# Optimization experiments

Hardware: AMD Instinct MI355X
Metric: run time of the kernel (lower is better)

The kernel has to match this reference:

```python
import jax, jax.numpy as jnp
import numpy as np

EPS = 1e-8  # torch cosine_similarity norm clamp


def _l2_normalize(x):
    # normalize last dim with torch-style eps clamp on the norm
    n = jnp.linalg.norm(x, axis=-1, keepdims=True)
    return x / jnp.maximum(n, EPS)


def setup_inputs() -> dict:
    key = jax.random.key(0)
    ks = jax.random.split(key, 6)
    T, Nq, D = 4, 4096, 1024
    Ns, H, P, C = 2048, 3, 256, 100
    return {
        "query_tube_feats": jax.random.normal(ks[0], (T, Nq, D), jnp.float32),
        "support_feats": jax.random.normal(ks[1], (Ns, D), jnp.float32),
        "head_W": jax.random.normal(ks[2], (H, D, P), jnp.float32) * (1.0 / np.sqrt(D)),
        "head_b": jax.random.normal(ks[3], (H, P), jnp.float32) * 0.01,
        "cls_W": jax.random.normal(ks[4], (D, C), jnp.float32) * (1.0 / np.sqrt(D)),
        "cls_b": jax.random.normal(ks[5], (C,), jnp.float32) * 0.01,
    }


def reference(query_tube_feats, support_feats, head_W, head_b, cls_W, cls_b):
    # aggregate_features with 'mean' aggregation over the tube/frame axis
    agg_query = jnp.mean(query_tube_feats, axis=0)                 # [Nq, D]

    # all 3 relation heads at once: Linear projections
    q = jnp.einsum('nd,hdp->hnp', agg_query, head_W) + head_b[:, None, :]   # [H, Nq, P]
    s = jnp.einsum('md,hdp->hmp', support_feats, head_W) + head_b[:, None, :]  # [H, Ns, P]

    # cosine similarity as fused normalize + GEMM (same math as broadcast cosine)
    qn = _l2_normalize(q)
    sn = _l2_normalize(s)
    dists = jnp.einsum('hnp,hmp->hnm', qn, sn)                     # [H, Nq, Ns]

    match_scores = jnp.mean(dists, axis=0)                         # [Nq, Ns]
    support_preds = support_feats @ cls_W + cls_b                  # [Ns, C]
    return match_scores, support_preds
```

## Files before the change

### kernel.cpp

```cpp
#include <hip/hip_runtime.h>

#define NQ 4096
#define NS 2048
#define DD 1024
#define HH 3
#define PP 256
#define CC 100
#define NR (NQ + NS)
#define PN (HH * PP)

typedef __attribute__((ext_vector_type(8))) short bf16x8;
typedef __attribute__((ext_vector_type(4))) float f32x4;

#define AS1 __attribute__((address_space(1)))
#define AS3 __attribute__((address_space(3)))

__device__ __forceinline__ void gload16(const void* g, void* l) {
  __builtin_amdgcn_global_load_lds((const AS1 unsigned int*)g,
                                   (AS3 unsigned int*)l, 16, 0, 0);
}

__device__ __forceinline__ unsigned short f2bf(float f) {
  union { float f; unsigned u; } v; v.f = f;
  return (unsigned short)((v.u + 0x7FFFu + ((v.u >> 16) & 1u)) >> 16);
}

__device__ __forceinline__ float bf2f(unsigned short s) {
  union { unsigned u; float f; } v; v.u = ((unsigned)s) << 16;
  return v.f;
}

__global__ __launch_bounds__(256) void prep_kernel(
    const float* __restrict__ q,
    const float* __restrict__ sup,
    const float* __restrict__ hW,
    const float* __restrict__ cW,
    unsigned short* __restrict__ Xq,
    unsigned short* __restrict__ Xs,
    unsigned short* __restrict__ Wt,
    unsigned short* __restrict__ WcT)
{
  __shared__ unsigned short T[64][72];
  const int b = blockIdx.x, t = threadIdx.x;

  if (b < 1536) {
    if (b < 1024) {
      #pragma unroll
      for (int i = 0; i < 4; ++i) {
        int idx = (b * 1024 + i * 256 + t) * 4;
        const float4 a  = *(const float4*)&q[idx];
        const float4 c1 = *(const float4*)&q[NQ * DD + idx];
        const float4 c2 = *(const float4*)&q[2 * NQ * DD + idx];
        const float4 c3 = *(const float4*)&q[3 * NQ * DD + idx];
        ushort4 o;
        o.x = f2bf((a.x + c1.x + c2.x + c3.x) * 0.25f);
        o.y = f2bf((a.y + c1.y + c2.y + c3.y) * 0.25f);
        o.z = f2bf((a.z + c1.z + c2.z + c3.z) * 0.25f);
        o.w = f2bf((a.w + c1.w + c2.w + c3.w) * 0.25f);
        *(ushort4*)&Xq[idx] = o;
      }
    } else {
      #pragma unroll
      for (int i = 0; i < 4; ++i) {
        int idx = ((b - 1024) * 1024 + i * 256 + t) * 4;
        const float4 a = *(const float4*)&sup[idx];
        ushort4 o;
        o.x = f2bf(a.x); o.y = f2bf(a.y); o.z = f2bf(a.z); o.w = f2bf(a.w);
        *(ushort4*)&Xs[idx] = o;
      }
    }
    return;
  }

  const float* src; unsigned short* dst; int srcC, pvalid, k0, p0;
  if (b < 1728) {
    int r = b - 1536; int h = r / 64; int rr = r % 64;
    k0 = (rr >> 2) * 64; p0 = (rr & 3) * 64;
    src = hW + h * DD * PP; srcC = PP; pvalid = PP;
    dst = Wt + (h * PP + p0) * DD;
  } else {
    int r = b - 1728;
    k0 = (r >> 1) * 64; p0 = (r & 1) * 64;
    src = cW; srcC = CC; pvalid = CC;
    dst = WcT + p0 * DD;
  }
  {
    int kl = t >> 2, pb = (t & 3) * 4;
    #pragma unroll
    for (int j = 0; j < 4; ++j) {
      int pl = pb + j * 16;
      int p = p0 + pl;
      float4 v; v.x = v.y = v.z = v.w = 0.f;
      if (p + 3 < pvalid) {
        v = *(const float4*)&src[(k0 + kl) * srcC + p];
      } else {
        if (p + 0 < pvalid) v.x = src[(k0 + kl) * srcC + p + 0];
        if (p + 1 < pvalid) v.y = src[(k0 + kl) * srcC + p + 1];
        if (p + 2 < pvalid) v.z = src[(k0 + kl) * srcC + p + 2];
        if (p + 3 < pvalid) v.w = src[(k0 + kl) * srcC + p + 3];
      }
      T[kl][pl + 0] = f2bf(v.x); T[kl][pl + 1] = f2bf(v.y);
      T[kl][pl + 2] = f2bf(v.z); T[kl][pl + 3] = f2bf(v.w);
    }
    __syncthreads();
    int pr = t >> 2, kb = (t & 3) * 4;
    #pragma unroll
    for (int j = 0; j < 4; ++j) {
      int kk = kb + j * 16;
      ushort4 o;
      o.x = T[kk + 0][pr]; o.y = T[kk + 1][pr];
      o.z = T[kk + 2][pr]; o.w = T[kk + 3][pr];
      *(ushort4*)&dst[pr * DD + k0 + kk] = o;
    }
  }
}

__global__ __launch_bounds__(256) void pgemm_kernel(
    const unsigned short* __restrict__ X,
    const unsigned short* __restrict__ Wall,
    const float* __restrict__ ball,
    unsigned short* __restrict__ QS)
{
  __shared__ __align__(16) char smem[65536];
  unsigned short* As = (unsigned short*)smem;
  unsigned short* Bs = (unsigned short*)(smem + 32768);
  unsigned short* Ct = (unsigned short*)smem;

  const int bid = blockIdx.x;
  const int swz = (bid & 7) * 36 + (bid >> 3);
  const int bm = swz / 6, bn = swz % 6;
  const int tid = threadIdx.x;
  const int w = tid >> 6, l = tid & 63;
  const int wm = w >> 1, wn = w & 1;
  const int rA = l & 15, kg = l >> 4;

  const unsigned short* A = X + bm * 128 * DD;
  const unsigned short* B = Wall + bn * 128 * DD;

  auto STAGE = [&](int buf, int kt) {
    #pragma unroll
    for (int i = 0; i < 8; ++i) {
      int c = w + i * 4;
      if (c < 16)
        gload16(A + (c * 8 + (l >> 3)) * DD + kt * 64 + (l & 7) * 8,
                &As[buf * 8192 + c * 512]);
      else
        gload16(B + ((c - 16) * 8 + (l >> 3)) * DD + kt * 64 + (l & 7) * 8,
                &Bs[buf * 8192 + (c - 16) * 512]);
    }
  };

  f32x4 acc[4][4] = {};
  STAGE(0, 0);
  __syncthreads();
  int cur = 0;
  for (int kt = 0; kt < DD / 64; ++kt) {
    if (kt + 1 < DD / 64) STAGE(cur ^ 1, kt + 1);
    #pragma unroll
    for (int kk = 0; kk < 2; ++kk) {
      bf16x8 a[4], bfr[4];
      #pragma unroll
      for (int mi = 0; mi < 4; ++mi)
        a[mi] = *(const bf16x8*)&As[cur * 8192 + (wm * 64 + mi * 16 + rA) * 64 + kk * 32 + kg * 8];
      #pragma unroll
      for (int ni = 0; ni < 4; ++ni)
        bfr[ni] = *(const bf16x8*)&Bs[cur * 8192 + (wn * 64 + ni * 16 + rA) * 64 + kk * 32 + kg * 8];
      #pragma unroll
      for (int mi = 0; mi < 4; ++mi)
        #pragma unroll
        for (int ni = 0; ni < 4; ++ni)
          acc[mi][ni] =
              __builtin_amdgcn_mfma_f32_16x16x32_bf16(a[mi], bfr[ni], acc[mi][ni], 0, 0, 0);
    }
    __syncthreads();
    cur ^= 1;
  }

  float bias[4];
  #pragma unroll
  for (int ni = 0; ni < 4; ++ni)
    bias[ni] = ball[bn * 128 + wn * 64 + ni * 16 + rA];

  #pragma unroll
  for (int mi = 0; mi < 4; ++mi)
    #pragma unroll
    for (int i = 0; i < 4; ++i) {
      int row = wm * 64 + mi * 16 + kg * 4 + i;
      #pragma unroll
      for (int ni = 0; ni < 4; ++ni)
        Ct[row * 136 + wn * 64 + ni * 16 + rA] = f2bf(acc[mi][ni][i] + bias[ni]);
    }
  __syncthreads();
  #pragma unroll
  for (int pass = 0; pass < 16; ++pass) {
    int row = pass * 8 + (tid >> 5);
    int c = tid & 31;
    ushort4 v = *(const ushort4*)&Ct[row * 136 + c * 4];
    *(ushort4*)&QS[(bm * 128 + row) * PN + bn * 128 + c * 4] = v;
  }
}

__global__ __launch_bounds__(256) void norm_kernel(
    unsigned short* __restrict__ QS)
{
  const int wid = blockIdx.x * 4 + (threadIdx.x >> 6);
  const int l = threadIdx.x & 63;
  unsigned short* rowp = QS + wid * PN;
  const float scale = (wid < NQ) ? (1.f / 3.f) : 1.f;

  float v[3][4];
  float ss[3];
  #pragma unroll
  for (int h = 0; h < 3; ++h) {
    ushort4 u = *(const ushort4*)&rowp[h * PP + l * 4];
    v[h][0] = bf2f(u.x); v[h][1] = bf2f(u.y);
    v[h][2] = bf2f(u.z); v[h][3] = bf2f(u.w);
    ss[h] = v[h][0]*v[h][0] + v[h][1]*v[h][1] + v[h][2]*v[h][2] + v[h][3]*v[h][3];
  }
  #pragma unroll
  for (int s = 1; s < 64; s <<= 1) {
    ss[0] += __shfl_xor(ss[0], s);
    ss[1] += __shfl_xor(ss[1], s);
    ss[2] += __shfl_xor(ss[2], s);
  }
  #pragma unroll
  for (int h = 0; h < 3; ++h) {
    float inv = scale / fmaxf(sqrtf(ss[h]), 1e-8f);
    ushort4 o;
    o.x = f2bf(v[h][0] * inv); o.y = f2bf(v[h][1] * inv);
    o.z = f2bf(v[h][2] * inv); o.w = f2bf(v[h][3] * inv);
    *(ushort4*)&rowp[h * PP + l * 4] = o;
  }
}

__global__ __launch_bounds__(256) void mm_kernel(
    const unsigned short* __restrict__ Qn,
    const unsigned short* __restrict__ Sn,
    const unsigned short* __restrict__ Xs,
    const unsigned short* __restrict__ WcT,
    const float* __restrict__ cb,
    float* __restrict__ out)
{
  __shared__ __align__(16) char smem[128 * 132 * 4];
  unsigned short* As = (unsigned short*)smem;
  unsigned short* Bs = (unsigned short*)(smem + 32768);
  float* Ct = (float*)smem;

  const int bid = blockIdx.x;
  const int tid = threadIdx.x;
  const int w = tid >> 6, l = tid & 63;
  const int wm = w >> 1, wn = w & 1;
  const int rA = l & 15, kg = l >> 4;

  const unsigned short *A, *B;
  int ldk, nkt, bm, bn;
  const bool match = bid < 512;
  if (match) {
    int xcd = bid & 7, idx = bid >> 3;
    bm = xcd * 4 + (idx & 3);
    bn = idx >> 2;
    A = Qn + bm * 128 * PN;
    B = Sn + bn * 128 * PN;
    ldk = PN; nkt = PN / 64;
  } else {
    bm = bid - 512; bn = 0;
    A = Xs + bm * 128 * DD;
    B = WcT;
    ldk = DD; nkt = DD / 64;
  }

  auto STAGE = [&](int buf, int kt) {
    #pragma unroll
    for (int i = 0; i < 8; ++i) {
      int c = w + i * 4;
      if (c < 16)
        gload16(A + (c * 8 + (l >> 3)) * ldk + kt * 64 + (l & 7) * 8,
                &As[buf * 8192 + c * 512]);
      else
        gload16(B + ((c - 16) * 8 + (l >> 3)) * ldk + kt * 64 + (l & 7) * 8,
                &Bs[buf * 8192 + (c - 16) * 512]);
    }
  };

  f32x4 acc[4][4] = {};
  STAGE(0, 0);
  __syncthreads();
  int cur = 0;
  for (int kt = 0; kt < nkt; ++kt) {
    if (kt + 1 < nkt) STAGE(cur ^ 1, kt + 1);
    #pragma unroll
    for (int kk = 0; kk < 2; ++kk) {
      bf16x8 a[4], bfr[4];
      #pragma unroll
      for (int mi = 0; mi < 4; ++mi)
        a[mi] = *(const bf16x8*)&As[cur * 8192 + (wm * 64 + mi * 16 + rA) * 64 + kk * 32 + kg * 8];
      #pragma unroll
      for (int ni = 0; ni < 4; ++ni)
        bfr[ni] = *(const bf16x8*)&Bs[cur * 8192 + (wn * 64 + ni * 16 + rA) * 64 + kk * 32 + kg * 8];
      #pragma unroll
      for (int mi = 0; mi < 4; ++mi)
        #pragma unroll
        for (int ni = 0; ni < 4; ++ni)
          acc[mi][ni] =
              __builtin_amdgcn_mfma_f32_16x16x32_bf16(a[mi], bfr[ni], acc[mi][ni], 0, 0, 0);
    }
    __syncthreads();
    cur ^= 1;
  }

  if (match) {
    #pragma unroll
    for (int mi = 0; mi < 4; ++mi)
      #pragma unroll
      for (int i = 0; i < 4; ++i) {
        int row = wm * 64 + mi * 16 + kg * 4 + i;
        #pragma unroll
        for (int ni = 0; ni < 4; ++ni)
          Ct[row * 132 + wn * 64 + ni * 16 + rA] = acc[mi][ni][i];
      }
    __syncthreads();
    #pragma unroll
    for (int pass = 0; pass < 16; ++pass) {
      int row = pass * 8 + (tid >> 5);
      int c = tid & 31;
      f32x4 v = *(const f32x4*)&Ct[row * 132 + c * 4];
      *(f32x4*)&out[(long)(bm * 128 + row) * NS + bn * 128 + c * 4] = v;
    }
  } else {
    float* o2 = out + (long)NQ * NS;
    #pragma unroll
    for (int mi = 0; mi < 4; ++mi)
      #pragma unroll
      for (int i = 0; i < 4; ++i) {
        int row = bm * 128 + wm * 64 + mi * 16 + kg * 4 + i;
        #pragma unroll
        for (int ni = 0; ni < 4; ++ni) {
          int col = wn * 64 + ni * 16 + rA;
          if (col < CC) o2[row * CC + col] = acc[mi][ni][i] + cb[col];
        }
      }
  }
}

extern "C" void kernel_launch(void* const* d_in, const int* in_sizes, int n_in,
                              void* d_out, int out_size, void* d_ws, size_t ws_size,
                              hipStream_t stream) {
  const float* q   = (const float*)d_in[0];
  const float* sup = (const float*)d_in[1];
  const float* hW  = (const float*)d_in[2];
  const float* hb  = (const float*)d_in[3];
  const float* cW  = (const float*)d_in[4];
  const float* cb  = (const float*)d_in[5];
  float* out = (float*)d_out;

  char* ws = (char*)d_ws;
  unsigned short* Xq  = (unsigned short*)(ws + 0);
  unsigned short* Xs  = (unsigned short*)(ws + (8u  << 20));
  unsigned short* Wt  = (unsigned short*)(ws + (12u << 20));
  unsigned short* WcT = (unsigned short*)(ws + (12u << 20) + 1572864u);
  unsigned short* QS  = (unsigned short*)(ws + (14u << 20));
  unsigned short* Qn  = QS;
  unsigned short* Sn  = QS + (size_t)NQ * PN;

  prep_kernel<<<1760, 256, 0, stream>>>(q, sup, hW, cW, Xq, Xs, Wt, WcT);
  pgemm_kernel<<<288, 256, 0, stream>>>(Xq, Wt, hb, QS);
  norm_kernel<<<NR / 4, 256, 0, stream>>>(QS);
  mm_kernel<<<512 + 16, 256, 0, stream>>>(Qn, Sn, Xs, WcT, cb, out);
}
```

Before: 181.7 us.

## XOR-swizzle LDS tiles and use explicit vmcnt waits for async pipelining

Both GEMM kernels now load global tiles into LDS with the column position XOR-swizzled by row, and read fragments back with the matching XOR. This is meant to remove LDS bank conflicts on the fragment reads. The loop also replaces __syncthreads with explicit s_waitcnt vmcnt(8) plus raw s_barrier, so the prefetch of the next tile can stay in flight while the current tile is consumed. The hand-placed waitcnt values depend on exactly eight loads per stage; if the count is wrong the kernel may read incomplete data.

```diff
diff --git a/kernel.cpp b/kernel.cpp
--- a/kernel.cpp
+++ b/kernel.cpp
@@ -14,6 +14,9 @@
 
 #define AS1 __attribute__((address_space(1)))
 #define AS3 __attribute__((address_space(3)))
+
+#define S_WAIT_VM(n) asm volatile("s_waitcnt vmcnt(" #n ")" ::: "memory")
+#define S_WAIT_LGKM0() asm volatile("s_waitcnt lgkmcnt(0)" ::: "memory")
 
 __device__ __forceinline__ void gload16(const void* g, void* l) {
   __builtin_amdgcn_global_load_lds((const AS1 unsigned int*)g,
@@ -133,6 +136,8 @@
   const int w = tid >> 6, l = tid & 63;
   const int wm = w >> 1, wn = w & 1;
   const int rA = l & 15, kg = l >> 4;
+  const int xr = (rA & 7) << 3;
+  const int colsw = ((l & 7) * 8) ^ ((l >> 3) << 3);
 
   const unsigned short* A = X + bm * 128 * DD;
   const unsigned short* B = Wall + bn * 128 * DD;
@@ -142,29 +147,37 @@
     for (int i = 0; i < 8; ++i) {
       int c = w + i * 4;
       if (c < 16)
-        gload16(A + (c * 8 + (l >> 3)) * DD + kt * 64 + (l & 7) * 8,
+        gload16(A + (c * 8 + (l >> 3)) * DD + kt * 64 + colsw,
                 &As[buf * 8192 + c * 512]);
       else
-        gload16(B + ((c - 16) * 8 + (l >> 3)) * DD + kt * 64 + (l & 7) * 8,
+        gload16(B + ((c - 16) * 8 + (l >> 3)) * DD + kt * 64 + colsw,
                 &Bs[buf * 8192 + (c - 16) * 512]);
     }
   };
 
   f32x4 acc[4][4] = {};
   STAGE(0, 0);
-  __syncthreads();
   int cur = 0;
   for (int kt = 0; kt < DD / 64; ++kt) {
-    if (kt + 1 < DD / 64) STAGE(cur ^ 1, kt + 1);
+    if (kt + 1 < DD / 64) {
+      STAGE(cur ^ 1, kt + 1);
+      S_WAIT_VM(8);
+    } else {
+      S_WAIT_VM(0);
+    }
+    __builtin_amdgcn_sched_barrier(0);
+    __builtin_amdgcn_s_barrier();
     #pragma unroll
     for (int kk = 0; kk < 2; ++kk) {
       bf16x8 a[4], bfr[4];
       #pragma unroll
       for (int mi = 0; mi < 4; ++mi)
-        a[mi] = *(const bf16x8*)&As[cur * 8192 + (wm * 64 + mi * 16 + rA) * 64 + kk * 32 + kg * 8];
+        a[mi] = *(const bf16x8*)&As[cur * 8192 + (wm * 64 + mi * 16 + rA) * 64 +
+                                    ((kk * 32 + kg * 8) ^ xr)];
       #pragma unroll
       for (int ni = 0; ni < 4; ++ni)
-        bfr[ni] = *(const bf16x8*)&Bs[cur * 8192 + (wn * 64 + ni * 16 + rA) * 64 + kk * 32 + kg * 8];
+        bfr[ni] = *(const bf16x8*)&Bs[cur * 8192 + (wn * 64 + ni * 16 + rA) * 64 +
+                                      ((kk * 32 + kg * 8) ^ xr)];
       #pragma unroll
       for (int mi = 0; mi < 4; ++mi)
         #pragma unroll
@@ -172,7 +185,9 @@
           acc[mi][ni] =
               __builtin_amdgcn_mfma_f32_16x16x32_bf16(a[mi], bfr[ni], acc[mi][ni], 0, 0, 0);
     }
-    __syncthreads();
+    S_WAIT_LGKM0();
+    __builtin_amdgcn_sched_barrier(0);
+    __builtin_amdgcn_s_barrier();
     cur ^= 1;
   }
 
@@ -251,6 +266,8 @@
   const int w = tid >> 6, l = tid & 63;
   const int wm = w >> 1, wn = w & 1;
   const int rA = l & 15, kg = l >> 4;
+  const int xr = (rA & 7) << 3;
+  const int colsw = ((l & 7) * 8) ^ ((l >> 3) << 3);
 
   const unsigned short *A, *B;
   int ldk, nkt, bm, bn;
@@ -274,29 +291,37 @@
     for (int i = 0; i < 8; ++i) {
       int c = w + i * 4;
       if (c < 16)
-        gload16(A + (c * 8 + (l >> 3)) * ldk + kt * 64 + (l & 7) * 8,
+        gload16(A + (c * 8 + (l >> 3)) * ldk + kt * 64 + colsw,
                 &As[buf * 8192 + c * 512]);
       else
-        gload16(B + ((c - 16) * 8 + (l >> 3)) * ldk + kt * 64 + (l & 7) * 8,
+        gload16(B + ((c - 16) * 8 + (l >> 3)) * ldk + kt * 64 + colsw,
                 &Bs[buf * 8192 + (c - 16) * 512]);
     }
   };
 
   f32x4 acc[4][4] = {};
   STAGE(0, 0);
-  __syncthreads();
   int cur = 0;
   for (int kt = 0; kt < nkt; ++kt) {
-    if (kt + 1 < nkt) STAGE(cur ^ 1, kt + 1);
+    if (kt + 1 < nkt) {
+      STAGE(cur ^ 1, kt + 1);
+      S_WAIT_VM(8);
+    } else {
+      S_WAIT_VM(0);
+    }
+    __builtin_amdgcn_sched_barrier(0);
+    __builtin_amdgcn_s_barrier();
     #pragma unroll
     for (int kk = 0; kk < 2; ++kk) {
       bf16x8 a[4], bfr[4];
       #pragma unroll
       for (int mi = 0; mi < 4; ++mi)
-        a[mi] = *(const bf16x8*)&As[cur * 8192 + (wm * 64 + mi * 16 + rA) * 64 + kk * 32 + kg * 8];
+        a[mi] = *(const bf16x8*)&As[cur * 8192 + (wm * 64 + mi * 16 + rA) * 64 +
+                                    ((kk * 32 + kg * 8) ^ xr)];
       #pragma unroll
       for (int ni = 0; ni < 4; ++ni)
-        bfr[ni] = *(const bf16x8*)&Bs[cur * 8192 + (wn * 64 + ni * 16 + rA) * 64 + kk * 32 + kg * 8];
+        bfr[ni] = *(const bf16x8*)&Bs[cur * 8192 + (wn * 64 + ni * 16 + rA) * 64 +
+                                      ((kk * 32 + kg * 8) ^ xr)];
       #pragma unroll
       for (int mi = 0; mi < 4; ++mi)
         #pragma unroll
@@ -304,7 +329,9 @@
           acc[mi][ni] =
               __builtin_amdgcn_mfma_f32_16x16x32_bf16(a[mi], bfr[ni], acc[mi][ni], 0, 0, 0);
     }
-    __syncthreads();
+    S_WAIT_LGKM0();
+    __builtin_amdgcn_sched_barrier(0);
+    __builtin_amdgcn_s_barrier();
     cur ^= 1;
   }
 
```

Result: faster. 171.5 us (-5.6%).
